# Optimization experiments

Hardware: AMD Instinct MI355X
Metric: run time of the kernel (lower is better)

The kernel has to match this reference:

```python
import jax, jax.numpy as jnp
import numpy as np

N, E, DIN, HID, DOUT = 50000, 800000, 128, 128, 64
NEG_SLOPE = 0.2


def setup_inputs() -> dict:
    key = jax.random.key(0)
    ks = jax.random.split(key, 16)
    x = jax.random.normal(ks[0], (N, DIN), dtype=jnp.float32)
    edge_index = jax.random.randint(ks[1], (2, E), 0, N, dtype=jnp.int64)

    def lin(k, fan_in, fan_out):
        kw, kb = jax.random.split(k)
        s = 1.0 / np.sqrt(fan_in)
        W = jax.random.uniform(kw, (fan_in, fan_out), jnp.float32, -s, s)
        b = jax.random.uniform(kb, (fan_out,), jnp.float32, -s, s)
        return W, b

    Wl, bl = lin(ks[2], DIN, DIN)   # GATv2 lin_l
    Wr, br = lin(ks[3], DIN, DIN)   # GATv2 lin_r
    att = jax.random.uniform(ks[4], (DIN,), jnp.float32, -1.0 / np.sqrt(DIN), 1.0 / np.sqrt(DIN))
    bg = jnp.zeros((DIN,), jnp.float32)  # GAT output bias
    W1, b1 = lin(ks[5], DIN, HID)   # ChebConv K=1 -> plain linear
    W2, b2 = lin(ks[6], HID, HID)
    W3, b3 = lin(ks[7], HID, DOUT)
    return {"x": x, "edge_index": edge_index, "Wl": Wl, "bl": bl, "Wr": Wr,
            "br": br, "att": att, "bg": bg, "W1": W1, "b1": b1,
            "W2": W2, "b2": b2, "W3": W3, "b3": b3}


def reference(x, edge_index, Wl, bl, Wr, br, att, bg, W1, b1, W2, b2, W3, b3):
    n = x.shape[0]
    # GATv2Conv adds self loops by default
    loop = jnp.arange(n, dtype=edge_index.dtype)
    src = jnp.concatenate([edge_index[0], loop])  # source j
    dst = jnp.concatenate([edge_index[1], loop])  # target i

    xl = x @ Wl + bl  # [N, DIN]
    xr = x @ Wr + br  # [N, DIN]

    # GATv2 edge scores: leaky_relu(x_l[j] + x_r[i]) . att
    e = jax.nn.leaky_relu(xl[src] + xr[dst], NEG_SLOPE)  # [E+N, DIN]
    a = e @ att                                          # [E+N]

    # softmax over incoming edges of each destination node
    amax = jax.ops.segment_max(a, dst, num_segments=n)
    ea = jnp.exp(a - amax[dst])
    denom = jax.ops.segment_sum(ea, dst, num_segments=n)
    alpha = ea / denom[dst]                              # [E+N]

    # aggregate messages alpha * x_l[j] at destinations
    h = jax.ops.segment_sum(alpha[:, None] * xl[src], dst, num_segments=n) + bg

    # ChebConv with K=1 reduces to a linear layer (T_0(L) = I)
    h = jax.nn.relu(h @ W1 + b1)
    h = jax.nn.relu(h @ W2 + b2)
    # dropout_rate = 0.0 -> identity
    return h @ W3 + b3
```

## Files before the change

### kernel.cpp

```cpp
#include <hip/hip_runtime.h>
#include <hip/hip_bf16.h>

#define DIN 128
#define NEG_SLOPE 0.2f
#define PTILE 2048
#define FCAP 8192
#define CVT_BLKS 289

typedef __attribute__((ext_vector_type(8))) short bf16x8;
typedef __attribute__((ext_vector_type(8))) unsigned short u16x8;
typedef __attribute__((ext_vector_type(4))) float f32x4;
typedef __attribute__((ext_vector_type(2))) float f32x2;
typedef __attribute__((ext_vector_type(4))) unsigned int u32x4;

__device__ __forceinline__ ushort f2bf(float f) {
  unsigned u = __float_as_uint(f);
  u += 0x7FFFu + ((u >> 16) & 1u);
  return (ushort)(u >> 16);
}
__device__ __forceinline__ float bf2f(ushort u) {
  return __uint_as_float((unsigned)u << 16);
}
__device__ __forceinline__ f32x2 bfpair(unsigned u) {
  f32x2 r;
  r.x = __uint_as_float(u << 16);
  r.y = __uint_as_float(u & 0xFFFF0000u);
  return r;
}

__global__ __launch_bounds__(256) void cvt_hist_kernel(
    const float* __restrict__ Wl, const float* __restrict__ Wr,
    const float* __restrict__ W1, const float* __restrict__ W2,
    const float* __restrict__ W3,
    ushort* __restrict__ WlT, ushort* __restrict__ WrT,
    ushort* __restrict__ W1T, ushort* __restrict__ W2T,
    ushort* __restrict__ W3T,
    const int* __restrict__ ei, int* __restrict__ ghist, int E) {
  if (blockIdx.x < CVT_BLKS) {
    int i = blockIdx.x * 256 + threadIdx.x;
    if (i < 16384) {
      int k = i >> 7, c = i & 127; WlT[c * 128 + k] = f2bf(Wl[i]);
    } else if (i < 32768) {
      int j = i - 16384; int k = j >> 7, c = j & 127; WrT[c * 128 + k] = f2bf(Wr[j]);
    } else if (i < 49152) {
      int j = i - 32768; int k = j >> 7, c = j & 127; W1T[c * 128 + k] = f2bf(W1[j]);
    } else if (i < 65536) {
      int j = i - 49152; int k = j >> 7, c = j & 127; W2T[c * 128 + k] = f2bf(W2[j]);
    } else if (i < 73728) {
      int j = i - 65536; int k = j >> 6, c = j & 63; W3T[c * 128 + k] = f2bf(W3[j]);
    }
  } else {
    __shared__ int h[256];
    h[threadIdx.x] = 0;
    __syncthreads();
    int tile = blockIdx.x - CVT_BLKS;
    for (int e = tile * PTILE + threadIdx.x;
         e < min(E, (tile + 1) * PTILE); e += 256)
      atomicAdd(&h[ei[E + e] >> 8], 1);
    __syncthreads();
    if (h[threadIdx.x] > 0) atomicAdd(&ghist[threadIdx.x], h[threadIdx.x]);
  }
}

__global__ __launch_bounds__(256) void scan_small_kernel(
    const int* __restrict__ ghist, int* __restrict__ cum,
    int* __restrict__ cursor) {
  __shared__ int sh[256];
  int tid = threadIdx.x;
  int v = ghist[tid];
  sh[tid] = v;
  __syncthreads();
  for (int d = 1; d < 256; d <<= 1) {
    int t = (tid >= d) ? sh[tid - d] : 0;
    __syncthreads();
    sh[tid] += t;
    __syncthreads();
  }
  int exc = sh[tid] - v;
  cum[tid] = exc;
  cursor[tid] = exc;
  if (tid == 255) cum[256] = sh[255];
}

__global__ __launch_bounds__(256) void lin_partition_kernel(
    const float* __restrict__ x,
    const ushort* __restrict__ WlT, const float* __restrict__ bl,
    const ushort* __restrict__ WrT, const float* __restrict__ br,
    ushort* __restrict__ xl, ushort* __restrict__ xr, int n, int nblk_lin,
    const int* __restrict__ ei, unsigned* __restrict__ part,
    int* __restrict__ cursor, int E) {
  if ((int)blockIdx.x < nblk_lin) {
    const int tid = threadIdx.x;
    const int wv = tid >> 6, lane = tid & 63;
    const int m = lane & 15, quad = lane >> 4;
    const int colbase = (wv & 1) * 64;
    const int nodew = blockIdx.x * 32 + (wv >> 1) * 16;
    int arow = nodew + m; if (arow >= n) arow = n - 1;
    f32x4 accl[4], accr[4];
#pragma unroll
    for (int nt = 0; nt < 4; nt++) { accl[nt] = (f32x4){0,0,0,0}; accr[nt] = (f32x4){0,0,0,0}; }
#pragma unroll
    for (int kk = 0; kk < 4; kk++) {
      int k0 = kk * 32 + quad * 8;
      const float4* xp = (const float4*)(x + (long)arow * 128 + k0);
      float4 x0 = xp[0], x1 = xp[1];
      bf16x8 af;
      af[0] = (short)f2bf(x0.x); af[1] = (short)f2bf(x0.y);
      af[2] = (short)f2bf(x0.z); af[3] = (short)f2bf(x0.w);
      af[4] = (short)f2bf(x1.x); af[5] = (short)f2bf(x1.y);
      af[6] = (short)f2bf(x1.z); af[7] = (short)f2bf(x1.w);
#pragma unroll
      for (int nt = 0; nt < 4; nt++) {
        int brow = colbase + nt * 16 + m;
        bf16x8 bl8 = *(const bf16x8*)(WlT + brow * 128 + k0);
        bf16x8 br8 = *(const bf16x8*)(WrT + brow * 128 + k0);
        accl[nt] = __builtin_amdgcn_mfma_f32_16x16x32_bf16(af, bl8, accl[nt], 0, 0, 0);
        accr[nt] = __builtin_amdgcn_mfma_f32_16x16x32_bf16(af, br8, accr[nt], 0, 0, 0);
      }
    }
#pragma unroll
    for (int nt = 0; nt < 4; nt++) {
      int col = colbase + nt * 16 + m;
      float vbl = bl[col], vbr = br[col];
#pragma unroll
      for (int r = 0; r < 4; r++) {
        int node = nodew + quad * 4 + r;
        if (node < n) {
          xl[(long)node * 128 + col] = f2bf(accl[nt][r] + vbl);
          xr[(long)node * 128 + col] = f2bf(accr[nt][r] + vbr);
        }
      }
    }
  } else {
    __shared__ int hist[256], pref[256], sexcl[256], curs[256], gbase[256];
    __shared__ unsigned buf[PTILE];
    const int tid = threadIdx.x;
    const int tile0 = ((int)blockIdx.x - nblk_lin) * PTILE;
    const int tcount = min(PTILE, E - tile0);
    hist[tid] = 0;
    __syncthreads();
    unsigned pk[PTILE / 256];
    int cnt = 0;
    for (int i = tid; i < tcount; i += 256) {
      int e = tile0 + i;
      int s = ei[e], d = ei[E + e];
      unsigned p = ((unsigned)d << 16) | (unsigned)s;
      pk[cnt++] = p;
      atomicAdd(&hist[d >> 8], 1);
    }
    __syncthreads();
    int v = hist[tid];
    pref[tid] = v;
    __syncthreads();
    for (int d = 1; d < 256; d <<= 1) {
      int t = (tid >= d) ? pref[tid - d] : 0;
      __syncthreads();
      pref[tid] += t;
      __syncthreads();
    }
    int exc = pref[tid] - v;
    sexcl[tid] = exc;
    curs[tid] = exc;
    gbase[tid] = (v > 0) ? atomicAdd(&cursor[tid], v) : 0;
    __syncthreads();
    for (int j = 0; j < cnt; j++) {
      int b = pk[j] >> 24;
      int pos = atomicAdd(&curs[b], 1);
      buf[pos] = pk[j];
    }
    __syncthreads();
    for (int i = tid; i < tcount; i += 256) {
      unsigned p = buf[i];
      int b = p >> 24;
      part[gbase[b] + (i - sexcl[b])] = p;
    }
  }
}

__global__ __launch_bounds__(512) void fine_kernel(
    const unsigned* __restrict__ part, const int* __restrict__ cum,
    int* __restrict__ offsets, ushort* __restrict__ ssrc,
    int N, int E, int nbuck) {
  __shared__ int hist[256], pref[256], curs[256];
  __shared__ unsigned buf[FCAP], buf2[FCAP];
  const int tid = threadIdx.x;
  const int b = blockIdx.x;
  const int seg0 = cum[b];
  const int len = min(cum[b + 1] - seg0, FCAP);
  if (tid < 256) hist[tid] = 0;
  __syncthreads();
  for (int i = tid; i < len; i += 512) {
    unsigned p = part[seg0 + i];
    buf[i] = p;
    atomicAdd(&hist[(p >> 16) & 255], 1);
  }
  __syncthreads();
  int v = (tid < 256) ? hist[tid] : 0;
  if (tid < 256) pref[tid] = v;
  __syncthreads();
  for (int d = 1; d < 256; d <<= 1) {
    int t = (tid >= d && tid < 256) ? pref[tid - d] : 0;
    __syncthreads();
    if (tid < 256) pref[tid] += t;
    __syncthreads();
  }
  if (tid < 256) {
    int exc = pref[tid] - v;
    curs[tid] = exc;
    int node = b * 256 + tid;
    if (node < N) offsets[node] = seg0 + exc;
  }
  if (b == nbuck - 1 && tid == 0) offsets[N] = E;
  __syncthreads();
  for (int i = tid; i < len; i += 512) {
    unsigned p = buf[i];
    int pos = atomicAdd(&curs[(p >> 16) & 255], 1);
    buf2[pos] = p;
  }
  __syncthreads();
  for (int i = tid; i < len; i += 512)
    ssrc[seg0 + i] = (ushort)(buf2[i] & 0xFFFFu);
}

__global__ __launch_bounds__(256) void node_aggr_kernel(
    const ushort* __restrict__ xl, const ushort* __restrict__ xr,
    const float* __restrict__ att, const float* __restrict__ bg,
    const int* __restrict__ offsets, const ushort* __restrict__ ssrc,
    ushort* __restrict__ h, int n) {
  int wave = (int)((blockIdx.x * (long)blockDim.x + threadIdx.x) >> 6);
  int lane = threadIdx.x & 63;
  if (wave >= n) return;
  const int node = wave;
  const int eg = lane >> 4, sl = lane & 15;
  f32x2 av2[4], r2[4], acc2[4];
  {
    const float4* ap = (const float4*)(att + sl * 8);
    float4 a0 = ap[0], a1 = ap[1];
    av2[0] = (f32x2){a0.x, a0.y}; av2[1] = (f32x2){a0.z, a0.w};
    av2[2] = (f32x2){a1.x, a1.y}; av2[3] = (f32x2){a1.z, a1.w};
  }
  u32x4 rv = *(const u32x4*)(xr + (long)node * 128 + sl * 8);
  u32x4 lv = *(const u32x4*)(xl + (long)node * 128 + sl * 8);
  float denom;
  {
    f32x2 t2 = {0.f, 0.f};
    f32x2 l2[4];
#pragma unroll
    for (int jp = 0; jp < 4; jp++) {
      r2[jp] = bfpair(rv[jp]);
      l2[jp] = bfpair(lv[jp]);
      f32x2 v = l2[jp] + r2[jp];
      t2 += __builtin_elementwise_max(v, NEG_SLOPE * v) * av2[jp];
    }
    float t = t2.x + t2.y;
#pragma unroll
    for (int off = 1; off < 16; off <<= 1) t += __shfl_xor(t, off);
    float es = __expf(t);
    denom = (eg == 0) ? es : 0.f;
#pragma unroll
    for (int jp = 0; jp < 4; jp++)
      acc2[jp] = (eg == 0) ? es * l2[jp] : (f32x2){0.f, 0.f};
  }
  const int beg = offsets[node];
  const int end = offsets[node + 1];
  for (int p = beg; p < end; p += 8) {
    int ia = p + 2 * eg;
    bool va = ia < end, vb = ia + 1 < end;
    int sa = va ? (int)ssrc[ia] : node;
    int sb = vb ? (int)ssrc[ia + 1] : node;
    u32x4 uva = *(const u32x4*)(xl + (long)sa * 128 + sl * 8);
    u32x4 uvb = *(const u32x4*)(xl + (long)sb * 128 + sl * 8);
    f32x2 ua2[4], ub2[4];
    f32x2 ta2 = {0.f, 0.f}, tb2 = {0.f, 0.f};
#pragma unroll
    for (int jp = 0; jp < 4; jp++) {
      ua2[jp] = bfpair(uva[jp]);
      ub2[jp] = bfpair(uvb[jp]);
      f32x2 va2 = ua2[jp] + r2[jp];
      f32x2 vb2 = ub2[jp] + r2[jp];
      ta2 += __builtin_elementwise_max(va2, NEG_SLOPE * va2) * av2[jp];
      tb2 += __builtin_elementwise_max(vb2, NEG_SLOPE * vb2) * av2[jp];
    }
    float ta = ta2.x + ta2.y, tb = tb2.x + tb2.y;
#pragma unroll
    for (int off = 1; off < 16; off <<= 1) {
      ta += __shfl_xor(ta, off);
      tb += __shfl_xor(tb, off);
    }
    float ea = va ? __expf(ta) : 0.f;
    float eb = vb ? __expf(tb) : 0.f;
    denom += ea + eb;
#pragma unroll
    for (int jp = 0; jp < 4; jp++)
      acc2[jp] += ea * ua2[jp] + eb * ub2[jp];
  }
#pragma unroll
  for (int jp = 0; jp < 4; jp++) {
    acc2[jp].x += __shfl_xor(acc2[jp].x, 16);
    acc2[jp].y += __shfl_xor(acc2[jp].y, 16);
    acc2[jp].x += __shfl_xor(acc2[jp].x, 32);
    acc2[jp].y += __shfl_xor(acc2[jp].y, 32);
  }
  denom += __shfl_xor(denom, 16);
  denom += __shfl_xor(denom, 32);
  if (eg == 0) {
    float inv = 1.0f / denom;
    const float4* bp = (const float4*)(bg + sl * 8);
    float4 g0 = bp[0], g1 = bp[1];
    f32x2 gv[4] = {{g0.x, g0.y}, {g0.z, g0.w}, {g1.x, g1.y}, {g1.z, g1.w}};
    u16x8 o;
#pragma unroll
    for (int jp = 0; jp < 4; jp++) {
      f32x2 hv = acc2[jp] * inv + gv[jp];
      o[2 * jp]     = f2bf(hv.x);
      o[2 * jp + 1] = f2bf(hv.y);
    }
    *(u16x8*)(h + (long)node * 128 + sl * 8) = o;
  }
}

#define LDSP 136
__global__ __launch_bounds__(256) void mlp_mfma_kernel(
    const ushort* __restrict__ hb,
    const ushort* __restrict__ W1T, const float* __restrict__ b1,
    const ushort* __restrict__ W2T, const float* __restrict__ b2,
    const ushort* __restrict__ W3T, const float* __restrict__ b3,
    float* __restrict__ out, int n) {
  __shared__ ushort act[32][LDSP];
  const int tid = threadIdx.x;
  const int wv = tid >> 6, lane = tid & 63;
  const int m = lane & 15, quad = lane >> 4;
  const int half = wv & 1, ng = wv >> 1;
  const int colbase = half * 64;
  const int nodew = blockIdx.x * 32 + ng * 16;
  int arow = nodew + m; if (arow >= n) arow = n - 1;
  f32x4 acc[4];
#pragma unroll
  for (int nt = 0; nt < 4; nt++) acc[nt] = (f32x4){0,0,0,0};
#pragma unroll
  for (int kk = 0; kk < 4; kk++) {
    int k0 = kk * 32 + quad * 8;
    bf16x8 af = *(const bf16x8*)(hb + (long)arow * 128 + k0);
#pragma unroll
    for (int nt = 0; nt < 4; nt++) {
      bf16x8 b8 = *(const bf16x8*)(W1T + (colbase + nt * 16 + m) * 128 + k0);
      acc[nt] = __builtin_amdgcn_mfma_f32_16x16x32_bf16(af, b8, acc[nt], 0, 0, 0);
    }
  }
#pragma unroll
  for (int nt = 0; nt < 4; nt++) {
    int col = colbase + nt * 16 + m;
    float b = b1[col];
#pragma unroll
    for (int r = 0; r < 4; r++)
      act[ng * 16 + quad * 4 + r][col] = f2bf(fmaxf(acc[nt][r] + b, 0.f));
  }
  __syncthreads();
#pragma unroll
  for (int nt = 0; nt < 4; nt++) acc[nt] = (f32x4){0,0,0,0};
#pragma unroll
  for (int kk = 0; kk < 4; kk++) {
    int k0 = kk * 32 + quad * 8;
    bf16x8 af = *(const bf16x8*)(&act[ng * 16 + m][k0]);
#pragma unroll
    for (int nt = 0; nt < 4; nt++) {
      bf16x8 b8 = *(const bf16x8*)(W2T + (colbase + nt * 16 + m) * 128 + k0);
      acc[nt] = __builtin_amdgcn_mfma_f32_16x16x32_bf16(af, b8, acc[nt], 0, 0, 0);
    }
  }
  __syncthreads();
#pragma unroll
  for (int nt = 0; nt < 4; nt++) {
    int col = colbase + nt * 16 + m;
    float b = b2[col];
#pragma unroll
    for (int r = 0; r < 4; r++)
      act[ng * 16 + quad * 4 + r][col] = f2bf(fmaxf(acc[nt][r] + b, 0.f));
  }
  __syncthreads();
  f32x4 acc3[2];
#pragma unroll
  for (int nt = 0; nt < 2; nt++) acc3[nt] = (f32x4){0,0,0,0};
#pragma unroll
  for (int kk = 0; kk < 4; kk++) {
    int k0 = kk * 32 + quad * 8;
    bf16x8 af = *(const bf16x8*)(&act[ng * 16 + m][k0]);
#pragma unroll
    for (int nt = 0; nt < 2; nt++) {
      bf16x8 b8 = *(const bf16x8*)(W3T + (half * 32 + nt * 16 + m) * 128 + k0);
      acc3[nt] = __builtin_amdgcn_mfma_f32_16x16x32_bf16(af, b8, acc3[nt], 0, 0, 0);
    }
  }
#pragma unroll
  for (int nt = 0; nt < 2; nt++) {
    int col = half * 32 + nt * 16 + m;
    float b = b3[col];
#pragma unroll
    for (int r = 0; r < 4; r++) {
      int node = nodew + quad * 4 + r;
      if (node < n) out[(long)node * 64 + col] = acc3[nt][r] + b;
    }
  }
}

extern "C" void kernel_launch(void* const* d_in, const int* in_sizes, int n_in,
                              void* d_out, int out_size, void* d_ws, size_t ws_size,
                              hipStream_t stream) {
  const float* x   = (const float*)d_in[0];
  const int*   ei  = (const int*)d_in[1];
  const float* Wl  = (const float*)d_in[2];
  const float* bl  = (const float*)d_in[3];
  const float* Wr  = (const float*)d_in[4];
  const float* br  = (const float*)d_in[5];
  const float* att = (const float*)d_in[6];
  const float* bg  = (const float*)d_in[7];
  const float* W1  = (const float*)d_in[8];
  const float* b1  = (const float*)d_in[9];
  const float* W2  = (const float*)d_in[10];
  const float* b2  = (const float*)d_in[11];
  const float* W3  = (const float*)d_in[12];
  const float* b3  = (const float*)d_in[13];
  float* out = (float*)d_out;

  const int N = in_sizes[0] / DIN;
  const int E = in_sizes[1] / 2;
  const int nbuck = (N + 255) >> 8;

  char* ws = (char*)d_ws;
  size_t off = 0;
  auto alloc = [&](size_t bytes) {
    void* p = ws + off;
    off += (bytes + 255) & ~(size_t)255;
    return p;
  };
  int* ghist     = (int*)alloc(256 * 4);
  int* cum       = (int*)alloc(257 * 4);
  int* cursor    = (int*)alloc(256 * 4);
  int* offsets   = (int*)alloc(((size_t)N + 4) * 4);
  unsigned* part = (unsigned*)alloc((size_t)E * 4);
  ushort* ssrc   = (ushort*)alloc(((size_t)E + 16) * 2);
  ushort* xlb    = (ushort*)alloc((size_t)N * DIN * 2);
  ushort* xrb    = (ushort*)alloc((size_t)N * DIN * 2);
  ushort* hbf    = (ushort*)alloc((size_t)N * DIN * 2);
  ushort* WlT    = (ushort*)alloc(16384 * 2);
  ushort* WrT    = (ushort*)alloc(16384 * 2);
  ushort* W1T    = (ushort*)alloc(16384 * 2);
  ushort* W2T    = (ushort*)alloc(16384 * 2);
  ushort* W3T    = (ushort*)alloc(8192 * 2);
  (void)ws_size;

  hipMemsetAsync(ghist, 0, 256 * 4, stream);

  int ntile = (E + PTILE - 1) / PTILE;
  cvt_hist_kernel<<<CVT_BLKS + ntile, 256, 0, stream>>>(
      Wl, Wr, W1, W2, W3, WlT, WrT, W1T, W2T, W3T, ei, ghist, E);

  scan_small_kernel<<<1, 256, 0, stream>>>(ghist, cum, cursor);

  int nblk32 = (N + 31) / 32;
  lin_partition_kernel<<<nblk32 + ntile, 256, 0, stream>>>(
      x, WlT, bl, WrT, br, xlb, xrb, N, nblk32, ei, part, cursor, E);

  fine_kernel<<<nbuck, 512, 0, stream>>>(part, cum, offsets, ssrc, N, E, nbuck);

  int nwblk = (N + 3) / 4;
  node_aggr_kernel<<<nwblk, 256, 0, stream>>>(xlb, xrb, att, bg,
                                              offsets, ssrc, hbf, N);

  mlp_mfma_kernel<<<nblk32, 256, 0, stream>>>(hbf, W1T, b1, W2T, b2,
                                              W3T, b3, out, N);
}
```

Before: 242.1 us.

## Fuse fine sort, attention aggregation and MLP into one kernel

```diff
diff --git a/kernel.cpp b/kernel.cpp
--- a/kernel.cpp
+++ b/kernel.cpp
@@ -4,8 +4,9 @@
 #define DIN 128
 #define NEG_SLOPE 0.2f
 #define PTILE 2048
-#define FCAP 8192
 #define CVT_BLKS 289
+#define SCAP 2560
+#define LDSP 136
 
 typedef __attribute__((ext_vector_type(8))) short bf16x8;
 typedef __attribute__((ext_vector_type(8))) unsigned short u16x8;
@@ -177,228 +178,233 @@
   }
 }
 
-__global__ __launch_bounds__(512) void fine_kernel(
-    const unsigned* __restrict__ part, const int* __restrict__ cum,
-    int* __restrict__ offsets, ushort* __restrict__ ssrc,
-    int N, int E, int nbuck) {
-  __shared__ int hist[256], pref[256], curs[256];
-  __shared__ unsigned buf[FCAP], buf2[FCAP];
-  const int tid = threadIdx.x;
-  const int b = blockIdx.x;
-  const int seg0 = cum[b];
-  const int len = min(cum[b + 1] - seg0, FCAP);
-  if (tid < 256) hist[tid] = 0;
-  __syncthreads();
-  for (int i = tid; i < len; i += 512) {
-    unsigned p = part[seg0 + i];
-    buf[i] = p;
-    atomicAdd(&hist[(p >> 16) & 255], 1);
-  }
-  __syncthreads();
-  int v = (tid < 256) ? hist[tid] : 0;
-  if (tid < 256) pref[tid] = v;
-  __syncthreads();
-  for (int d = 1; d < 256; d <<= 1) {
-    int t = (tid >= d && tid < 256) ? pref[tid - d] : 0;
-    __syncthreads();
-    if (tid < 256) pref[tid] += t;
-    __syncthreads();
-  }
-  if (tid < 256) {
-    int exc = pref[tid] - v;
-    curs[tid] = exc;
-    int node = b * 256 + tid;
-    if (node < N) offsets[node] = seg0 + exc;
-  }
-  if (b == nbuck - 1 && tid == 0) offsets[N] = E;
-  __syncthreads();
-  for (int i = tid; i < len; i += 512) {
-    unsigned p = buf[i];
-    int pos = atomicAdd(&curs[(p >> 16) & 255], 1);
-    buf2[pos] = p;
-  }
-  __syncthreads();
-  for (int i = tid; i < len; i += 512)
-    ssrc[seg0 + i] = (ushort)(buf2[i] & 0xFFFFu);
-}
-
-__global__ __launch_bounds__(256) void node_aggr_kernel(
+__global__ __launch_bounds__(256) void aggr_mlp_kernel(
     const ushort* __restrict__ xl, const ushort* __restrict__ xr,
     const float* __restrict__ att, const float* __restrict__ bg,
-    const int* __restrict__ offsets, const ushort* __restrict__ ssrc,
-    ushort* __restrict__ h, int n) {
-  int wave = (int)((blockIdx.x * (long)blockDim.x + threadIdx.x) >> 6);
-  int lane = threadIdx.x & 63;
-  if (wave >= n) return;
-  const int node = wave;
+    const unsigned* __restrict__ part, const int* __restrict__ cum,
+    const ushort* __restrict__ W1T, const float* __restrict__ b1,
+    const ushort* __restrict__ W2T, const float* __restrict__ b2,
+    const ushort* __restrict__ W3T, const float* __restrict__ b3,
+    float* __restrict__ out, int n) {
+  __shared__ int hist[64], offs[65], curs[64];
+  __shared__ ushort ssrc[SCAP];
+  __shared__ ushort hbuf[64][LDSP];
+  const int tid = threadIdx.x;
+  const int b = blockIdx.x >> 2, sub = blockIdx.x & 3;
+  const int node_lo = (b << 8) + (sub << 6);
+  const int dlo = node_lo, dhi = node_lo + 64;
+  const int seg0 = cum[b];
+  const int len = cum[b + 1] - seg0;
+
+  if (tid < 64) hist[tid] = 0;
+  __syncthreads();
+  for (int i = tid; i < len; i += 256) {
+    int d = (int)(part[seg0 + i] >> 16);
+    if (d >= dlo && d < dhi) atomicAdd(&hist[d - dlo], 1);
+  }
+  __syncthreads();
+  if (tid < 64) {
+    int v = hist[tid];
+    int s = v;
+#pragma unroll
+    for (int dd = 1; dd < 64; dd <<= 1) {
+      int t = __shfl_up(s, dd);
+      if (tid >= dd) s += t;
+    }
+    offs[tid] = s - v;
+    curs[tid] = s - v;
+    if (tid == 63) offs[64] = s;
+  }
+  __syncthreads();
+  for (int i = tid; i < len; i += 256) {
+    unsigned p = part[seg0 + i];
+    int d = (int)(p >> 16);
+    if (d >= dlo && d < dhi) {
+      int pos = atomicAdd(&curs[d - dlo], 1);
+      if (pos < SCAP) ssrc[pos] = (ushort)(p & 0xFFFFu);
+    }
+  }
+  __syncthreads();
+
+  const int wv = tid >> 6, lane = tid & 63;
   const int eg = lane >> 4, sl = lane & 15;
-  f32x2 av2[4], r2[4], acc2[4];
+  f32x2 av2[4], gv2[4];
   {
     const float4* ap = (const float4*)(att + sl * 8);
     float4 a0 = ap[0], a1 = ap[1];
     av2[0] = (f32x2){a0.x, a0.y}; av2[1] = (f32x2){a0.z, a0.w};
     av2[2] = (f32x2){a1.x, a1.y}; av2[3] = (f32x2){a1.z, a1.w};
-  }
-  u32x4 rv = *(const u32x4*)(xr + (long)node * 128 + sl * 8);
-  u32x4 lv = *(const u32x4*)(xl + (long)node * 128 + sl * 8);
-  float denom;
-  {
-    f32x2 t2 = {0.f, 0.f};
-    f32x2 l2[4];
-#pragma unroll
-    for (int jp = 0; jp < 4; jp++) {
-      r2[jp] = bfpair(rv[jp]);
-      l2[jp] = bfpair(lv[jp]);
-      f32x2 v = l2[jp] + r2[jp];
-      t2 += __builtin_elementwise_max(v, NEG_SLOPE * v) * av2[jp];
-    }
-    float t = t2.x + t2.y;
-#pragma unroll
-    for (int off = 1; off < 16; off <<= 1) t += __shfl_xor(t, off);
-    float es = __expf(t);
-    denom = (eg == 0) ? es : 0.f;
-#pragma unroll
-    for (int jp = 0; jp < 4; jp++)
-      acc2[jp] = (eg == 0) ? es * l2[jp] : (f32x2){0.f, 0.f};
-  }
-  const int beg = offsets[node];
-  const int end = offsets[node + 1];
-  for (int p = beg; p < end; p += 8) {
-    int ia = p + 2 * eg;
-    bool va = ia < end, vb = ia + 1 < end;
-    int sa = va ? (int)ssrc[ia] : node;
-    int sb = vb ? (int)ssrc[ia + 1] : node;
-    u32x4 uva = *(const u32x4*)(xl + (long)sa * 128 + sl * 8);
-    u32x4 uvb = *(const u32x4*)(xl + (long)sb * 128 + sl * 8);
-    f32x2 ua2[4], ub2[4];
-    f32x2 ta2 = {0.f, 0.f}, tb2 = {0.f, 0.f};
-#pragma unroll
-    for (int jp = 0; jp < 4; jp++) {
-      ua2[jp] = bfpair(uva[jp]);
-      ub2[jp] = bfpair(uvb[jp]);
-      f32x2 va2 = ua2[jp] + r2[jp];
-      f32x2 vb2 = ub2[jp] + r2[jp];
-      ta2 += __builtin_elementwise_max(va2, NEG_SLOPE * va2) * av2[jp];
-      tb2 += __builtin_elementwise_max(vb2, NEG_SLOPE * vb2) * av2[jp];
-    }
-    float ta = ta2.x + ta2.y, tb = tb2.x + tb2.y;
-#pragma unroll
-    for (int off = 1; off < 16; off <<= 1) {
-      ta += __shfl_xor(ta, off);
-      tb += __shfl_xor(tb, off);
-    }
-    float ea = va ? __expf(ta) : 0.f;
-    float eb = vb ? __expf(tb) : 0.f;
-    denom += ea + eb;
-#pragma unroll
-    for (int jp = 0; jp < 4; jp++)
-      acc2[jp] += ea * ua2[jp] + eb * ub2[jp];
-  }
-#pragma unroll
-  for (int jp = 0; jp < 4; jp++) {
-    acc2[jp].x += __shfl_xor(acc2[jp].x, 16);
-    acc2[jp].y += __shfl_xor(acc2[jp].y, 16);
-    acc2[jp].x += __shfl_xor(acc2[jp].x, 32);
-    acc2[jp].y += __shfl_xor(acc2[jp].y, 32);
-  }
-  denom += __shfl_xor(denom, 16);
-  denom += __shfl_xor(denom, 32);
-  if (eg == 0) {
-    float inv = 1.0f / denom;
     const float4* bp = (const float4*)(bg + sl * 8);
     float4 g0 = bp[0], g1 = bp[1];
-    f32x2 gv[4] = {{g0.x, g0.y}, {g0.z, g0.w}, {g1.x, g1.y}, {g1.z, g1.w}};
-    u16x8 o;
+    gv2[0] = (f32x2){g0.x, g0.y}; gv2[1] = (f32x2){g0.z, g0.w};
+    gv2[2] = (f32x2){g1.x, g1.y}; gv2[3] = (f32x2){g1.z, g1.w};
+  }
+  for (int t = 0; t < 16; t++) {
+    const int ln = (wv << 4) + t;
+    const int node = node_lo + ln;
+    if (node >= n) {
+      if (eg == 0) {
+        u16x8 z;
+#pragma unroll
+        for (int j = 0; j < 8; j++) z[j] = 0;
+        *(u16x8*)(&hbuf[ln][sl * 8]) = z;
+      }
+      continue;
+    }
+    f32x2 r2[4], acc2[4];
+    u32x4 rv = *(const u32x4*)(xr + (long)node * 128 + sl * 8);
+    u32x4 lv = *(const u32x4*)(xl + (long)node * 128 + sl * 8);
+    float denom;
+    {
+      f32x2 t2 = {0.f, 0.f};
+      f32x2 l2[4];
+#pragma unroll
+      for (int jp = 0; jp < 4; jp++) {
+        r2[jp] = bfpair(rv[jp]);
+        l2[jp] = bfpair(lv[jp]);
+        f32x2 v = l2[jp] + r2[jp];
+        t2 += __builtin_elementwise_max(v, NEG_SLOPE * v) * av2[jp];
+      }
+      float tt = t2.x + t2.y;
+#pragma unroll
+      for (int off = 1; off < 16; off <<= 1) tt += __shfl_xor(tt, off);
+      float es = __expf(tt);
+      denom = (eg == 0) ? es : 0.f;
+#pragma unroll
+      for (int jp = 0; jp < 4; jp++)
+        acc2[jp] = (eg == 0) ? es * l2[jp] : (f32x2){0.f, 0.f};
+    }
+    const int beg = min(offs[ln], SCAP);
+    const int end = min(offs[ln + 1], SCAP);
+    for (int p = beg; p < end; p += 8) {
+      int ia = p + 2 * eg;
+      bool va = ia < end, vb = ia + 1 < end;
+      int sa = va ? (int)ssrc[ia] : node;
+      int sb = vb ? (int)ssrc[ia + 1] : node;
+      u32x4 uva = *(const u32x4*)(xl + (long)sa * 128 + sl * 8);
+      u32x4 uvb = *(const u32x4*)(xl + (long)sb * 128 + sl * 8);
+      f32x2 ua2[4], ub2[4];
+      f32x2 ta2 = {0.f, 0.f}, tb2 = {0.f, 0.f};
+#pragma unroll
+      for (int jp = 0; jp < 4; jp++) {
+        ua2[jp] = bfpair(uva[jp]);
+        ub2[jp] = bfpair(uvb[jp]);
+        f32x2 va2 = ua2[jp] + r2[jp];
+        f32x2 vb2 = ub2[jp] + r2[jp];
+        ta2 += __builtin_elementwise_max(va2, NEG_SLOPE * va2) * av2[jp];
+        tb2 += __builtin_elementwise_max(vb2, NEG_SLOPE * vb2) * av2[jp];
+      }
+      float ta = ta2.x + ta2.y, tb = tb2.x + tb2.y;
+#pragma unroll
+      for (int off = 1; off < 16; off <<= 1) {
+        ta += __shfl_xor(ta, off);
+        tb += __shfl_xor(tb, off);
+      }
+      float ea = va ? __expf(ta) : 0.f;
+      float eb = vb ? __expf(tb) : 0.f;
+      denom += ea + eb;
+#pragma unroll
+      for (int jp = 0; jp < 4; jp++)
+        acc2[jp] += ea * ua2[jp] + eb * ub2[jp];
+    }
 #pragma unroll
     for (int jp = 0; jp < 4; jp++) {
-      f32x2 hv = acc2[jp] * inv + gv[jp];
-      o[2 * jp]     = f2bf(hv.x);
-      o[2 * jp + 1] = f2bf(hv.y);
-    }
-    *(u16x8*)(h + (long)node * 128 + sl * 8) = o;
-  }
-}
-
-#define LDSP 136
-__global__ __launch_bounds__(256) void mlp_mfma_kernel(
-    const ushort* __restrict__ hb,
-    const ushort* __restrict__ W1T, const float* __restrict__ b1,
-    const ushort* __restrict__ W2T, const float* __restrict__ b2,
-    const ushort* __restrict__ W3T, const float* __restrict__ b3,
-    float* __restrict__ out, int n) {
-  __shared__ ushort act[32][LDSP];
-  const int tid = threadIdx.x;
-  const int wv = tid >> 6, lane = tid & 63;
+      acc2[jp].x += __shfl_xor(acc2[jp].x, 16);
+      acc2[jp].y += __shfl_xor(acc2[jp].y, 16);
+      acc2[jp].x += __shfl_xor(acc2[jp].x, 32);
+      acc2[jp].y += __shfl_xor(acc2[jp].y, 32);
+    }
+    denom += __shfl_xor(denom, 16);
+    denom += __shfl_xor(denom, 32);
+    if (eg == 0) {
+      float inv = 1.0f / denom;
+      u16x8 o;
+#pragma unroll
+      for (int jp = 0; jp < 4; jp++) {
+        f32x2 hv = acc2[jp] * inv + gv2[jp];
+        o[2 * jp]     = f2bf(hv.x);
+        o[2 * jp + 1] = f2bf(hv.y);
+      }
+      *(u16x8*)(&hbuf[ln][sl * 8]) = o;
+    }
+  }
+  __syncthreads();
+
   const int m = lane & 15, quad = lane >> 4;
-  const int half = wv & 1, ng = wv >> 1;
-  const int colbase = half * 64;
-  const int nodew = blockIdx.x * 32 + ng * 16;
-  int arow = nodew + m; if (arow >= n) arow = n - 1;
-  f32x4 acc[4];
-#pragma unroll
-  for (int nt = 0; nt < 4; nt++) acc[nt] = (f32x4){0,0,0,0};
+  const int arow = (wv << 4) + m;
+  bf16x8 af[4];
+  f32x4 acc[8];
+#pragma unroll
+  for (int kk = 0; kk < 4; kk++)
+    af[kk] = *(const bf16x8*)(&hbuf[arow][kk * 32 + quad * 8]);
+#pragma unroll
+  for (int nt = 0; nt < 8; nt++) acc[nt] = (f32x4){0,0,0,0};
 #pragma unroll
   for (int kk = 0; kk < 4; kk++) {
     int k0 = kk * 32 + quad * 8;
-    bf16x8 af = *(const bf16x8*)(hb + (long)arow * 128 + k0);
-#pragma unroll
-    for (int nt = 0; nt < 4; nt++) {
-      bf16x8 b8 = *(const bf16x8*)(W1T + (colbase + nt * 16 + m) * 128 + k0);
-      acc[nt] = __builtin_amdgcn_mfma_f32_16x16x32_bf16(af, b8, acc[nt], 0, 0, 0);
-    }
-  }
-#pragma unroll
-  for (int nt = 0; nt < 4; nt++) {
-    int col = colbase + nt * 16 + m;
-    float b = b1[col];
+#pragma unroll
+    for (int nt = 0; nt < 8; nt++) {
+      bf16x8 b8 = *(const bf16x8*)(W1T + (nt * 16 + m) * 128 + k0);
+      acc[nt] = __builtin_amdgcn_mfma_f32_16x16x32_bf16(af[kk], b8, acc[nt], 0, 0, 0);
+    }
+  }
+  __syncthreads();
+#pragma unroll
+  for (int nt = 0; nt < 8; nt++) {
+    int col = nt * 16 + m;
+    float bv = b1[col];
 #pragma unroll
     for (int r = 0; r < 4; r++)
-      act[ng * 16 + quad * 4 + r][col] = f2bf(fmaxf(acc[nt][r] + b, 0.f));
-  }
-  __syncthreads();
-#pragma unroll
-  for (int nt = 0; nt < 4; nt++) acc[nt] = (f32x4){0,0,0,0};
+      hbuf[(wv << 4) + quad * 4 + r][col] = f2bf(fmaxf(acc[nt][r] + bv, 0.f));
+  }
+  __syncthreads();
+#pragma unroll
+  for (int kk = 0; kk < 4; kk++)
+    af[kk] = *(const bf16x8*)(&hbuf[arow][kk * 32 + quad * 8]);
+#pragma unroll
+  for (int nt = 0; nt < 8; nt++) acc[nt] = (f32x4){0,0,0,0};
 #pragma unroll
   for (int kk = 0; kk < 4; kk++) {
     int k0 = kk * 32 + quad * 8;
-    bf16x8 af = *(const bf16x8*)(&act[ng * 16 + m][k0]);
-#pragma unroll
-    for (int nt = 0; nt < 4; nt++) {
-      bf16x8 b8 = *(const bf16x8*)(W2T + (colbase + nt * 16 + m) * 128 + k0);
-      acc[nt] = __builtin_amdgcn_mfma_f32_16x16x32_bf16(af, b8, acc[nt], 0, 0, 0);
-    }
-  }
-  __syncthreads();
-#pragma unroll
-  for (int nt = 0; nt < 4; nt++) {
-    int col = colbase + nt * 16 + m;
-    float b = b2[col];
+#pragma unroll
+    for (int nt = 0; nt < 8; nt++) {
+      bf16x8 b8 = *(const bf16x8*)(W2T + (nt * 16 + m) * 128 + k0);
+      acc[nt] = __builtin_amdgcn_mfma_f32_16x16x32_bf16(af[kk], b8, acc[nt], 0, 0, 0);
+    }
+  }
+  __syncthreads();
+#pragma unroll
+  for (int nt = 0; nt < 8; nt++) {
+    int col = nt * 16 + m;
+    float bv = b2[col];
 #pragma unroll
     for (int r = 0; r < 4; r++)
-      act[ng * 16 + quad * 4 + r][col] = f2bf(fmaxf(acc[nt][r] + b, 0.f));
-  }
-  __syncthreads();
-  f32x4 acc3[2];
-#pragma unroll
-  for (int nt = 0; nt < 2; nt++) acc3[nt] = (f32x4){0,0,0,0};
+      hbuf[(wv << 4) + quad * 4 + r][col] = f2bf(fmaxf(acc[nt][r] + bv, 0.f));
+  }
+  __syncthreads();
+#pragma unroll
+  for (int kk = 0; kk < 4; kk++)
+    af[kk] = *(const bf16x8*)(&hbuf[arow][kk * 32 + quad * 8]);
+  f32x4 acc3[4];
+#pragma unroll
+  for (int nt = 0; nt < 4; nt++) acc3[nt] = (f32x4){0,0,0,0};
 #pragma unroll
   for (int kk = 0; kk < 4; kk++) {
     int k0 = kk * 32 + quad * 8;
-    bf16x8 af = *(const bf16x8*)(&act[ng * 16 + m][k0]);
-#pragma unroll
-    for (int nt = 0; nt < 2; nt++) {
-      bf16x8 b8 = *(const bf16x8*)(W3T + (half * 32 + nt * 16 + m) * 128 + k0);
-      acc3[nt] = __builtin_amdgcn_mfma_f32_16x16x32_bf16(af, b8, acc3[nt], 0, 0, 0);
-    }
-  }
-#pragma unroll
-  for (int nt = 0; nt < 2; nt++) {
-    int col = half * 32 + nt * 16 + m;
-    float b = b3[col];
+#pragma unroll
+    for (int nt = 0; nt < 4; nt++) {
+      bf16x8 b8 = *(const bf16x8*)(W3T + (nt * 16 + m) * 128 + k0);
+      acc3[nt] = __builtin_amdgcn_mfma_f32_16x16x32_bf16(af[kk], b8, acc3[nt], 0, 0, 0);
+    }
+  }
+#pragma unroll
+  for (int nt = 0; nt < 4; nt++) {
+    int col = nt * 16 + m;
+    float bv = b3[col];
 #pragma unroll
     for (int r = 0; r < 4; r++) {
-      int node = nodew + quad * 4 + r;
-      if (node < n) out[(long)node * 64 + col] = acc3[nt][r] + b;
+      int node = node_lo + (wv << 4) + quad * 4 + r;
+      if (node < n) out[(long)node * 64 + col] = acc3[nt][r] + bv;
     }
   }
 }
@@ -436,12 +442,9 @@
   int* ghist     = (int*)alloc(256 * 4);
   int* cum       = (int*)alloc(257 * 4);
   int* cursor    = (int*)alloc(256 * 4);
-  int* offsets   = (int*)alloc(((size_t)N + 4) * 4);
   unsigned* part = (unsigned*)alloc((size_t)E * 4);
-  ushort* ssrc   = (ushort*)alloc(((size_t)E + 16) * 2);
   ushort* xlb    = (ushort*)alloc((size_t)N * DIN * 2);
   ushort* xrb    = (ushort*)alloc((size_t)N * DIN * 2);
-  ushort* hbf    = (ushort*)alloc((size_t)N * DIN * 2);
   ushort* WlT    = (ushort*)alloc(16384 * 2);
   ushort* WrT    = (ushort*)alloc(16384 * 2);
   ushort* W1T    = (ushort*)alloc(16384 * 2);
@@ -461,12 +464,6 @@
   lin_partition_kernel<<<nblk32 + ntile, 256, 0, stream>>>(
       x, WlT, bl, WrT, br, xlb, xrb, N, nblk32, ei, part, cursor, E);
 
-  fine_kernel<<<nbuck, 512, 0, stream>>>(part, cum, offsets, ssrc, N, E, nbuck);
-
-  int nwblk = (N + 3) / 4;
-  node_aggr_kernel<<<nwblk, 256, 0, stream>>>(xlb, xrb, att, bg,
-                                              offsets, ssrc, hbf, N);
-
-  mlp_mfma_kernel<<<nblk32, 256, 0, stream>>>(hbf, W1T, b1, W2T, b2,
-                                              W3T, b3, out, N);
-}
+  aggr_mlp_kernel<<<nbuck * 4, 256, 0, stream>>>(
+      xlb, xrb, att, bg, part, cum, W1T, b1, W2T, b2, W3T, b3, out, N);
+}
```

Measured after the change: 294.0 us. +21.4%, slower.
